# Kernel optimization log

Hardware: AMD Instinct MI355X
Metric: run time of the kernel (lower is better)

The kernel has to match this reference:

```python
import jax, jax.numpy as jnp
import numpy as np

C = 64
CK = C // 8  # query/key channels


def setup_inputs() -> dict:
    key = jax.random.key(0)
    ks = jax.random.split(key, 8)
    b, c, h, w = 4, C, 64, 64
    x = jax.random.normal(ks[0], (b, c, h, w), dtype=jnp.float32)
    # 1x1 conv weights (spectral-normalized weights are still just dense weights at eval)
    wq = jax.random.normal(ks[1], (CK, c), dtype=jnp.float32) * 0.05
    bq = jax.random.normal(ks[2], (CK,), dtype=jnp.float32) * 0.01
    wk = jax.random.normal(ks[3], (CK, c), dtype=jnp.float32) * 0.05
    bk = jax.random.normal(ks[4], (CK,), dtype=jnp.float32) * 0.01
    wv = jax.random.normal(ks[5], (c, c), dtype=jnp.float32) * 0.05
    bv = jax.random.normal(ks[6], (c,), dtype=jnp.float32) * 0.01
    # gamma is initialized to 0 in the module; use a nonzero value so the
    # attention path contributes to the output.
    gamma = jax.random.normal(ks[7], (1,), dtype=jnp.float32) * 0.5
    return {"x": x, "wq": wq, "bq": bq, "wk": wk, "bk": bk,
            "wv": wv, "bv": bv, "gamma": gamma}


def reference(x, wq, bq, wk, bk, wv, bv, gamma):
    b, c, h, w = x.shape
    n = h * w
    xf = x.reshape(b, c, n)                      # [b, c, n]
    # 1x1 convs as matmuls over the channel dim
    q = jnp.einsum('oc,bcn->bno', wq, xf) + bq   # [b, n, ck]
    k = jnp.einsum('oc,bcn->bon', wk, xf) + bk[None, :, None]  # [b, ck, n]
    v = jnp.einsum('oc,bcn->bno', wv, xf) + bv   # [b, n, c]
    attn = jax.nn.softmax(jnp.einsum('bnd,bdm->bnm', q, k), axis=-1)  # [b, n, n]
    o = jnp.einsum('bnm,bmc->bnc', attn, v)      # [b, n, c]
    o = o.transpose(0, 2, 1).reshape(b, c, h, w)
    return gamma[0] * o + x
```

## Files before the change

kernel.cpp:

```cpp
#include <hip/hip_runtime.h>
#include <hip/hip_bf16.h>

#define CH 64
#define NN 4096
#define NB 4
#define SPLIT 8
#define KLEN (NN / SPLIT)
#define VSTRIDE 520
#define LOG2E 1.44269504f

typedef unsigned short u16;
typedef unsigned int u32;
typedef __attribute__((ext_vector_type(8))) short bf16x8;
typedef __attribute__((ext_vector_type(16))) float f32x16;

static __device__ __forceinline__ u16 bf16r(float f) {
  union { float f; unsigned u; } v; v.f = f;
  unsigned x = v.u;
  x += 0x7fffu + ((x >> 16) & 1u);
  return (u16)(x >> 16);
}
static __device__ __forceinline__ u32 pkc(float a, float b) {
  union { __hip_bfloat162 h; u32 u; } r;
  r.h = __float22bfloat162_rn(float2{a, b});
  return r.u;
}

__global__ __launch_bounds__(192) void prep_w(
    const float* __restrict__ wq, const float* __restrict__ wk,
    const float* __restrict__ wv, u16* __restrict__ Afr) {
  for (int idx = threadIdx.x; idx < 768; idx += 192) {
    const int l = idx & 63;
    const int s = (idx >> 6) & 3;
    const int t = idx >> 8;
    const int row = 32 * t + (l & 31);
    const int c0 = 16 * s + 8 * (l >> 5);
    float e[8];
#pragma unroll
    for (int j = 0; j < 8; ++j) {
      float v = 0.f;
      if (row < 64)      v = wv[row * 64 + c0 + j];
      else if (row < 72) v = wq[(row - 64) * 64 + c0 + j];
      else if (row < 80) v = wk[(row - 72) * 64 + c0 + j];
      e[j] = v;
    }
    u32* dst = reinterpret_cast<u32*>(Afr + (size_t)idx * 8);
    dst[0] = pkc(e[0], e[1]); dst[1] = pkc(e[2], e[3]);
    dst[2] = pkc(e[4], e[5]); dst[3] = pkc(e[6], e[7]);
  }
}

__global__ __launch_bounds__(192) void qkv_proj(
    const float* __restrict__ x, const u16* __restrict__ Afr,
    const float* __restrict__ bq, const float* __restrict__ bk,
    const float* __restrict__ bv,
    u16* __restrict__ Qb, u16* __restrict__ Kb, u16* __restrict__ Vb) {
  __shared__ float xs[64 * 32];
  const int tid = threadIdx.x;
  const int b = blockIdx.x >> 7;
  const int n0 = (blockIdx.x & 127) << 5;

  const float* xbase = x + (size_t)b * CH * NN + n0;
  for (int i = tid; i < 512; i += 192) {
    const int row = i >> 3, c4 = i & 7;
    *reinterpret_cast<float4*>(&xs[row * 32 + c4 * 4]) =
        *reinterpret_cast<const float4*>(xbase + (size_t)row * NN + c4 * 4);
  }
  __syncthreads();

  const int w = __builtin_amdgcn_readfirstlane(tid >> 6);
  const int lane = tid & 63;
  const int l31 = lane & 31;
  const int h = lane >> 5;
  const int n = n0 + l31;

  f32x16 acc = {};
#pragma unroll
  for (int s = 0; s < 4; ++s) {
    const bf16x8 af = *reinterpret_cast<const bf16x8*>(
        Afr + ((size_t)(w * 4 + s) * 64 + lane) * 8);
    float xv[8];
#pragma unroll
    for (int j = 0; j < 8; ++j)
      xv[j] = xs[(16 * s + 8 * h + j) * 32 + l31];
    union { uint4 u; bf16x8 v; } bf;
    bf.u.x = pkc(xv[0], xv[1]); bf.u.y = pkc(xv[2], xv[3]);
    bf.u.z = pkc(xv[4], xv[5]); bf.u.w = pkc(xv[6], xv[7]);
    acc = __builtin_amdgcn_mfma_f32_32x32x16_bf16(af, bf.v, acc, 0, 0, 0);
  }

  if (w < 2) {
    const int sperm = (l31 & 19) | ((l31 & 4) << 1) | ((l31 & 8) >> 1);
    const int nperm = n0 + sperm;
#pragma unroll
    for (int r = 0; r < 16; ++r) {
      const int row = 32 * w + (r & 3) + 8 * (r >> 2) + 4 * h;
      Vb[((size_t)b * CH + row) * NN + nperm] = bf16r(acc[r] + bv[row]);
    }
  } else {
    const float q0 = (acc[0] + bq[4 * h + 0]) * LOG2E;
    const float q1 = (acc[1] + bq[4 * h + 1]) * LOG2E;
    const float q2 = (acc[2] + bq[4 * h + 2]) * LOG2E;
    const float q3 = (acc[3] + bq[4 * h + 3]) * LOG2E;
    const float k0 = acc[4] + bk[4 * h + 0];
    const float k1 = acc[5] + bk[4 * h + 1];
    const float k2 = acc[6] + bk[4 * h + 2];
    const float k3 = acc[7] + bk[4 * h + 3];
    uint2 qv, kv;
    qv.x = pkc(q0, q1); qv.y = pkc(q2, q3);
    kv.x = pkc(k0, k1); kv.y = pkc(k2, k3);
    *reinterpret_cast<uint2*>(Qb + ((size_t)b * NN + n) * 8 + 4 * h) = qv;
    *reinterpret_cast<uint2*>(Kb + ((size_t)b * NN + n) * 8 + 4 * h) = kv;
  }
}

__global__ __launch_bounds__(1024, 4) void flash_attn(
    const u16* __restrict__ Qb, const u16* __restrict__ Kb,
    const u16* __restrict__ Vb, u32* __restrict__ ACCu,
    float* __restrict__ Lb) {
  __shared__ u16 Klds[KLEN * 8 + 8];
  __shared__ u16 Vlds[64 * VSTRIDE];
  const int bid = blockIdx.x;
  const int sp = bid & 7;
  const int rest = bid >> 3;
  const int qc = rest & 7;
  const int b = rest >> 3;
  const int w = __builtin_amdgcn_readfirstlane(threadIdx.x >> 6);
  const int lane = threadIdx.x & 63;
  const int l31 = lane & 31;
  const int h = lane >> 5;
  const int qrow0 = qc * 512 + w * 32;
  const int ks = sp * KLEN;

  if (threadIdx.x < 8) Klds[KLEN * 8 + threadIdx.x] = 0;

  bf16x8 qf = {0, 0, 0, 0, 0, 0, 0, 0};
  if (h == 0)
    qf = *reinterpret_cast<const bf16x8*>(Qb + ((size_t)b * NN + qrow0 + l31) * 8);

  const u16* Kp = Kb + ((size_t)b * NN + ks) * 8;
  const u16* Vp = Vb + (size_t)b * CH * NN + ks;

#pragma unroll
  for (int i = 0; i < 4; ++i) {
    const int ch = 4 * w + i;
    const int m = (ch ^ (ch >> 3)) & 7;
    const u16* src = Vp + (size_t)ch * NN + (((lane & 56) | ((lane ^ m) & 7)) << 3);
    __builtin_amdgcn_global_load_lds(
        (const __attribute__((address_space(1))) void*)src,
        (__attribute__((address_space(3))) void*)&Vlds[ch * VSTRIDE], 16, 0, 0);
  }
  if (w < 8)
    __builtin_amdgcn_global_load_lds(
        (const __attribute__((address_space(1))) void*)(Kp + ((size_t)(64 * w + lane)) * 8),
        (__attribute__((address_space(3))) void*)&Klds[64 * w * 8], 16, 0, 0);
  __syncthreads();

  f32x16 acc0 = {}, acc1 = {}, acc2 = {};
  const f32x16 zz = {};
  const short one = (short)0x3F80;
  const bf16x8 zero8 = {0, 0, 0, 0, 0, 0, 0, 0};
  const bf16x8 ones8 = {one, one, one, one, one, one, one, one};
  const bf16x8 af1 = (l31 == 0) ? ones8 : zero8;
  const int m0 = (l31 ^ (l31 >> 3)) & 7;
  const int m1 = m0 ^ 4;

#pragma unroll 4
  for (int kk = 0; kk < KLEN / 32; ++kk) {
    const int kaddr = h ? KLEN * 8 : (kk * 32 + l31) * 8;
    bf16x8 kf = *reinterpret_cast<const bf16x8*>(Klds + kaddr);
    f32x16 s = __builtin_amdgcn_mfma_f32_32x32x16_bf16(kf, qf, zz, 0, 0, 0);
    float p[16];
#pragma unroll
    for (int r = 0; r < 16; ++r) p[r] = exp2f(s[r]);
    union { uint4 u; bf16x8 v; } pb0, pb1;
    pb0.u.x = pkc(p[0], p[1]);   pb0.u.y = pkc(p[2], p[3]);
    pb0.u.z = pkc(p[4], p[5]);   pb0.u.w = pkc(p[6], p[7]);
    pb1.u.x = pkc(p[8], p[9]);   pb1.u.y = pkc(p[10], p[11]);
    pb1.u.z = pkc(p[12], p[13]); pb1.u.w = pkc(p[14], p[15]);
    const int g0 = kk * 4 + h;
    const int g1 = g0 + 2;
    const int cp00 = (g0 & 56) | ((g0 ^ m0) & 7);
    const int cp01 = (g1 & 56) | ((g1 ^ m0) & 7);
    const int cp10 = (g0 & 56) | ((g0 ^ m1) & 7);
    const int cp11 = (g1 & 56) | ((g1 ^ m1) & 7);
    bf16x8 v00 = *reinterpret_cast<const bf16x8*>(Vlds + l31 * VSTRIDE + cp00 * 8);
    bf16x8 v01 = *reinterpret_cast<const bf16x8*>(Vlds + l31 * VSTRIDE + cp01 * 8);
    bf16x8 v10 = *reinterpret_cast<const bf16x8*>(Vlds + (32 + l31) * VSTRIDE + cp10 * 8);
    bf16x8 v11 = *reinterpret_cast<const bf16x8*>(Vlds + (32 + l31) * VSTRIDE + cp11 * 8);
    acc0 = __builtin_amdgcn_mfma_f32_32x32x16_bf16(v00, pb0.v, acc0, 0, 0, 0);
    acc0 = __builtin_amdgcn_mfma_f32_32x32x16_bf16(v01, pb1.v, acc0, 0, 0, 0);
    acc1 = __builtin_amdgcn_mfma_f32_32x32x16_bf16(v10, pb0.v, acc1, 0, 0, 0);
    acc1 = __builtin_amdgcn_mfma_f32_32x32x16_bf16(v11, pb1.v, acc1, 0, 0, 0);
    acc2 = __builtin_amdgcn_mfma_f32_32x32x16_bf16(af1, pb0.v, acc2, 0, 0, 0);
    acc2 = __builtin_amdgcn_mfma_f32_32x32x16_bf16(af1, pb1.v, acc2, 0, 0, 0);
  }

  float lsum = acc2[0];
  lsum += __shfl_xor(lsum, 32);

  const int gtile = b * (NN / 32) + qc * 16 + w;
  u32* A = ACCu + ((size_t)gtile * SPLIT + sp) * 32 * 32;
#pragma unroll
  for (int rp = 0; rp < 8; ++rp) {
    const int chp = (rp & 1) + 4 * (rp >> 1) + 2 * h;
    __builtin_nontemporal_store(pkc(acc0[2 * rp], acc0[2 * rp + 1]),
                                &A[chp * 32 + l31]);
    __builtin_nontemporal_store(pkc(acc1[2 * rp], acc1[2 * rp + 1]),
                                &A[(16 + chp) * 32 + l31]);
  }
  if (h == 0)
    __builtin_nontemporal_store(lsum, &Lb[((size_t)gtile * SPLIT + sp) * 32 + l31]);
}

__global__ __launch_bounds__(256) void combine(
    const float* __restrict__ x, const float* __restrict__ gamma,
    const u32* __restrict__ ACCu, const float* __restrict__ Lb,
    float* __restrict__ out) {
  const int idx = blockIdx.x * 256 + threadIdx.x;
  const int n4 = idx & (NN / 4 - 1);
  const int cp = (idx >> 10) & 31;
  const int b = idx >> 15;
  const int n = n4 << 2;
  const int gtile = b * (NN / 32) + (n >> 5);
  const int q0 = n & 31;
  const uint4* A4 = reinterpret_cast<const uint4*>(ACCu);
  const float4* L4 = reinterpret_cast<const float4*>(Lb);
  float s0[4] = {0.f, 0.f, 0.f, 0.f}, s1[4] = {0.f, 0.f, 0.f, 0.f};
  float l[4] = {0.f, 0.f, 0.f, 0.f};
#pragma unroll
  for (int sp = 0; sp < SPLIT; ++sp) {
    const uint4 a = A4[(((size_t)gtile * SPLIT + sp) * 32 + cp) * 8 + (q0 >> 2)];
    const float4 lv = L4[(((size_t)gtile * SPLIT + sp) * 32 + q0) >> 2];
    const u32 av[4] = {a.x, a.y, a.z, a.w};
#pragma unroll
    for (int k = 0; k < 4; ++k) {
      union { u32 u; float f; } lo, hi;
      lo.u = av[k] << 16; hi.u = av[k] & 0xffff0000u;
      s0[k] += lo.f; s1[k] += hi.f;
    }
    l[0] += lv.x; l[1] += lv.y; l[2] += lv.z; l[3] += lv.w;
  }
  const float gm = gamma[0];
  float inv[4];
#pragma unroll
  for (int k = 0; k < 4; ++k) inv[k] = gm / l[k];
  const size_t i0 = ((size_t)b * CH + 2 * cp) * NN + n;
  const float4 x0 = *reinterpret_cast<const float4*>(x + i0);
  const float4 x1 = *reinterpret_cast<const float4*>(x + i0 + NN);
  float4 o0, o1;
  o0.x = fmaf(inv[0], s0[0], x0.x); o0.y = fmaf(inv[1], s0[1], x0.y);
  o0.z = fmaf(inv[2], s0[2], x0.z); o0.w = fmaf(inv[3], s0[3], x0.w);
  o1.x = fmaf(inv[0], s1[0], x1.x); o1.y = fmaf(inv[1], s1[1], x1.y);
  o1.z = fmaf(inv[2], s1[2], x1.z); o1.w = fmaf(inv[3], s1[3], x1.w);
  *reinterpret_cast<float4*>(out + i0) = o0;
  *reinterpret_cast<float4*>(out + i0 + NN) = o1;
}

extern "C" void kernel_launch(void* const* d_in, const int* in_sizes, int n_in,
                              void* d_out, int out_size, void* d_ws, size_t ws_size,
                              hipStream_t stream) {
  const float* x     = (const float*)d_in[0];
  const float* wq    = (const float*)d_in[1];
  const float* bq    = (const float*)d_in[2];
  const float* wk    = (const float*)d_in[3];
  const float* bk    = (const float*)d_in[4];
  const float* wv    = (const float*)d_in[5];
  const float* bv    = (const float*)d_in[6];
  const float* gamma = (const float*)d_in[7];
  float* out = (float*)d_out;

  u16* Qb = (u16*)d_ws;
  u16* Kb = Qb + (size_t)NB * NN * 8;
  u16* Vb = Kb + (size_t)NB * NN * 8;
  u32* ACCu = (u32*)(Vb + (size_t)NB * CH * NN);
  float* Lb = (float*)(ACCu + (size_t)NB * (NN / 32) * SPLIT * 32 * 32);
  u16* Afr = (u16*)(Lb + (size_t)NB * (NN / 32) * SPLIT * 32);

  prep_w<<<dim3(1), dim3(192), 0, stream>>>(wq, wk, wv, Afr);
  qkv_proj<<<dim3(NB * (NN / 32)), dim3(192), 0, stream>>>(
      x, Afr, bq, bk, bv, Qb, Kb, Vb);
  flash_attn<<<dim3(NB * 8 * SPLIT), dim3(1024), 0, stream>>>(
      Qb, Kb, Vb, ACCu, Lb);
  combine<<<dim3((NB * 32 * (NN / 4)) / 256), dim3(256), 0, stream>>>(
      x, gamma, ACCu, Lb, out);
}
```

Before: 115.6 us.

## Halve key split and stream keys through LDS in two phases per block

Result: faster. 112.4 us (-2.8%).

```diff
diff --git a/kernel.cpp b/kernel.cpp
--- a/kernel.cpp
+++ b/kernel.cpp
@@ -4,8 +4,9 @@
 #define CH 64
 #define NN 4096
 #define NB 4
-#define SPLIT 8
+#define SPLIT 4
 #define KLEN (NN / SPLIT)
+#define PHK 512
 #define VSTRIDE 520
 #define LOG2E 1.44269504f
 
@@ -114,25 +115,25 @@
   }
 }
 
-__global__ __launch_bounds__(1024, 4) void flash_attn(
+__global__ __launch_bounds__(512, 4) void flash_attn(
     const u16* __restrict__ Qb, const u16* __restrict__ Kb,
     const u16* __restrict__ Vb, u32* __restrict__ ACCu,
     float* __restrict__ Lb) {
-  __shared__ u16 Klds[KLEN * 8 + 8];
+  __shared__ u16 Klds[PHK * 8 + 8];
   __shared__ u16 Vlds[64 * VSTRIDE];
   const int bid = blockIdx.x;
-  const int sp = bid & 7;
-  const int rest = bid >> 3;
-  const int qc = rest & 7;
-  const int b = rest >> 3;
+  const int sp = bid & 3;
+  const int rest = bid >> 2;
+  const int qc = rest & 15;
+  const int b = rest >> 4;
   const int w = __builtin_amdgcn_readfirstlane(threadIdx.x >> 6);
   const int lane = threadIdx.x & 63;
   const int l31 = lane & 31;
   const int h = lane >> 5;
-  const int qrow0 = qc * 512 + w * 32;
+  const int qrow0 = qc * 256 + w * 32;
   const int ks = sp * KLEN;
 
-  if (threadIdx.x < 8) Klds[KLEN * 8 + threadIdx.x] = 0;
+  if (threadIdx.x < 8) Klds[PHK * 8 + threadIdx.x] = 0;
 
   bf16x8 qf = {0, 0, 0, 0, 0, 0, 0, 0};
   if (h == 0)
@@ -140,21 +141,6 @@
 
   const u16* Kp = Kb + ((size_t)b * NN + ks) * 8;
   const u16* Vp = Vb + (size_t)b * CH * NN + ks;
-
-#pragma unroll
-  for (int i = 0; i < 4; ++i) {
-    const int ch = 4 * w + i;
-    const int m = (ch ^ (ch >> 3)) & 7;
-    const u16* src = Vp + (size_t)ch * NN + (((lane & 56) | ((lane ^ m) & 7)) << 3);
-    __builtin_amdgcn_global_load_lds(
-        (const __attribute__((address_space(1))) void*)src,
-        (__attribute__((address_space(3))) void*)&Vlds[ch * VSTRIDE], 16, 0, 0);
-  }
-  if (w < 8)
-    __builtin_amdgcn_global_load_lds(
-        (const __attribute__((address_space(1))) void*)(Kp + ((size_t)(64 * w + lane)) * 8),
-        (__attribute__((address_space(3))) void*)&Klds[64 * w * 8], 16, 0, 0);
-  __syncthreads();
 
   f32x16 acc0 = {}, acc1 = {}, acc2 = {};
   const f32x16 zz = {};
@@ -165,41 +151,64 @@
   const int m0 = (l31 ^ (l31 >> 3)) & 7;
   const int m1 = m0 ^ 4;
 
+#define STAGE(ph) do {                                                        \
+    _Pragma("unroll")                                                         \
+    for (int i = 0; i < 8; ++i) {                                             \
+      const int ch = 8 * w + i;                                               \
+      const int mm = (ch ^ (ch >> 3)) & 7;                                    \
+      const u16* src = Vp + (size_t)ch * NN + (ph) * PHK +                    \
+                       (((lane & 56) | ((lane ^ mm) & 7)) << 3);              \
+      __builtin_amdgcn_global_load_lds(                                       \
+          (const __attribute__((address_space(1))) void*)src,                 \
+          (__attribute__((address_space(3))) void*)&Vlds[ch * VSTRIDE], 16, 0, 0); \
+    }                                                                         \
+    __builtin_amdgcn_global_load_lds(                                         \
+        (const __attribute__((address_space(1))) void*)(Kp + ((size_t)(ph) * PHK + 64 * w + lane) * 8), \
+        (__attribute__((address_space(3))) void*)&Klds[64 * w * 8], 16, 0, 0); \
+  } while (0)
+
+#pragma unroll
+  for (int ph = 0; ph < 2; ++ph) {
+    STAGE(ph);
+    __syncthreads();
 #pragma unroll 4
-  for (int kk = 0; kk < KLEN / 32; ++kk) {
-    const int kaddr = h ? KLEN * 8 : (kk * 32 + l31) * 8;
-    bf16x8 kf = *reinterpret_cast<const bf16x8*>(Klds + kaddr);
-    f32x16 s = __builtin_amdgcn_mfma_f32_32x32x16_bf16(kf, qf, zz, 0, 0, 0);
-    float p[16];
-#pragma unroll
-    for (int r = 0; r < 16; ++r) p[r] = exp2f(s[r]);
-    union { uint4 u; bf16x8 v; } pb0, pb1;
-    pb0.u.x = pkc(p[0], p[1]);   pb0.u.y = pkc(p[2], p[3]);
-    pb0.u.z = pkc(p[4], p[5]);   pb0.u.w = pkc(p[6], p[7]);
-    pb1.u.x = pkc(p[8], p[9]);   pb1.u.y = pkc(p[10], p[11]);
-    pb1.u.z = pkc(p[12], p[13]); pb1.u.w = pkc(p[14], p[15]);
-    const int g0 = kk * 4 + h;
-    const int g1 = g0 + 2;
-    const int cp00 = (g0 & 56) | ((g0 ^ m0) & 7);
-    const int cp01 = (g1 & 56) | ((g1 ^ m0) & 7);
-    const int cp10 = (g0 & 56) | ((g0 ^ m1) & 7);
-    const int cp11 = (g1 & 56) | ((g1 ^ m1) & 7);
-    bf16x8 v00 = *reinterpret_cast<const bf16x8*>(Vlds + l31 * VSTRIDE + cp00 * 8);
-    bf16x8 v01 = *reinterpret_cast<const bf16x8*>(Vlds + l31 * VSTRIDE + cp01 * 8);
-    bf16x8 v10 = *reinterpret_cast<const bf16x8*>(Vlds + (32 + l31) * VSTRIDE + cp10 * 8);
-    bf16x8 v11 = *reinterpret_cast<const bf16x8*>(Vlds + (32 + l31) * VSTRIDE + cp11 * 8);
-    acc0 = __builtin_amdgcn_mfma_f32_32x32x16_bf16(v00, pb0.v, acc0, 0, 0, 0);
-    acc0 = __builtin_amdgcn_mfma_f32_32x32x16_bf16(v01, pb1.v, acc0, 0, 0, 0);
-    acc1 = __builtin_amdgcn_mfma_f32_32x32x16_bf16(v10, pb0.v, acc1, 0, 0, 0);
-    acc1 = __builtin_amdgcn_mfma_f32_32x32x16_bf16(v11, pb1.v, acc1, 0, 0, 0);
-    acc2 = __builtin_amdgcn_mfma_f32_32x32x16_bf16(af1, pb0.v, acc2, 0, 0, 0);
-    acc2 = __builtin_amdgcn_mfma_f32_32x32x16_bf16(af1, pb1.v, acc2, 0, 0, 0);
-  }
+    for (int kk = 0; kk < PHK / 32; ++kk) {
+      const int kaddr = h ? PHK * 8 : (kk * 32 + l31) * 8;
+      bf16x8 kf = *reinterpret_cast<const bf16x8*>(Klds + kaddr);
+      f32x16 s = __builtin_amdgcn_mfma_f32_32x32x16_bf16(kf, qf, zz, 0, 0, 0);
+      float p[16];
+#pragma unroll
+      for (int r = 0; r < 16; ++r) p[r] = exp2f(s[r]);
+      union { uint4 u; bf16x8 v; } pb0, pb1;
+      pb0.u.x = pkc(p[0], p[1]);   pb0.u.y = pkc(p[2], p[3]);
+      pb0.u.z = pkc(p[4], p[5]);   pb0.u.w = pkc(p[6], p[7]);
+      pb1.u.x = pkc(p[8], p[9]);   pb1.u.y = pkc(p[10], p[11]);
+      pb1.u.z = pkc(p[12], p[13]); pb1.u.w = pkc(p[14], p[15]);
+      const int g0 = kk * 4 + h;
+      const int g1 = g0 + 2;
+      const int cp00 = (g0 & 56) | ((g0 ^ m0) & 7);
+      const int cp01 = (g1 & 56) | ((g1 ^ m0) & 7);
+      const int cp10 = (g0 & 56) | ((g0 ^ m1) & 7);
+      const int cp11 = (g1 & 56) | ((g1 ^ m1) & 7);
+      bf16x8 v00 = *reinterpret_cast<const bf16x8*>(Vlds + l31 * VSTRIDE + cp00 * 8);
+      bf16x8 v01 = *reinterpret_cast<const bf16x8*>(Vlds + l31 * VSTRIDE + cp01 * 8);
+      bf16x8 v10 = *reinterpret_cast<const bf16x8*>(Vlds + (32 + l31) * VSTRIDE + cp10 * 8);
+      bf16x8 v11 = *reinterpret_cast<const bf16x8*>(Vlds + (32 + l31) * VSTRIDE + cp11 * 8);
+      acc0 = __builtin_amdgcn_mfma_f32_32x32x16_bf16(v00, pb0.v, acc0, 0, 0, 0);
+      acc0 = __builtin_amdgcn_mfma_f32_32x32x16_bf16(v01, pb1.v, acc0, 0, 0, 0);
+      acc1 = __builtin_amdgcn_mfma_f32_32x32x16_bf16(v10, pb0.v, acc1, 0, 0, 0);
+      acc1 = __builtin_amdgcn_mfma_f32_32x32x16_bf16(v11, pb1.v, acc1, 0, 0, 0);
+      acc2 = __builtin_amdgcn_mfma_f32_32x32x16_bf16(af1, pb0.v, acc2, 0, 0, 0);
+      acc2 = __builtin_amdgcn_mfma_f32_32x32x16_bf16(af1, pb1.v, acc2, 0, 0, 0);
+    }
+    if (ph == 0) __syncthreads();
+  }
+#undef STAGE
 
   float lsum = acc2[0];
   lsum += __shfl_xor(lsum, 32);
 
-  const int gtile = b * (NN / 32) + qc * 16 + w;
+  const int gtile = b * (NN / 32) + qc * 8 + w;
   u32* A = ACCu + ((size_t)gtile * SPLIT + sp) * 32 * 32;
 #pragma unroll
   for (int rp = 0; rp < 8; ++rp) {
@@ -280,7 +289,7 @@
   prep_w<<<dim3(1), dim3(192), 0, stream>>>(wq, wk, wv, Afr);
   qkv_proj<<<dim3(NB * (NN / 32)), dim3(192), 0, stream>>>(
       x, Afr, bq, bk, bv, Qb, Kb, Vb);
-  flash_attn<<<dim3(NB * 8 * SPLIT), dim3(1024), 0, stream>>>(
+  flash_attn<<<dim3(NB * 16 * SPLIT), dim3(512), 0, stream>>>(
       Qb, Kb, Vb, ACCu, Lb);
   combine<<<dim3((NB * 32 * (NN / 4)) / 256), dim3(256), 0, stream>>>(
       x, gamma, ACCu, Lb, out);
```
